# Kernel optimization log

Hardware: AMD Instinct MI355X
Metric: run time of the kernel (lower is better)

The kernel has to match this reference:

```python
import jax, jax.numpy as jnp
import numpy as np

N_NODES = 50000
N_EDGES = 800000
NF = 128   # node feature dim
EF = 64    # edge feature dim
H = 256    # hidden width (make_nn default [256, 256])
EO = 128   # edge_out_features
NO = 128   # node_out_features


def setup_inputs() -> dict:
    key = jax.random.key(0)
    ks = jax.random.split(key, 12)

    def w(k, fan_in, fan_out):
        return jax.random.normal(k, (fan_in, fan_out), jnp.float32) / np.float32(np.sqrt(fan_in))

    return {
        "node_attrs": jax.random.normal(ks[0], (N_NODES, NF), jnp.float32),
        "edge_attrs": jax.random.normal(ks[1], (N_EDGES, EF), jnp.float32),
        "senders": jax.random.randint(ks[2], (N_EDGES,), 0, N_NODES),
        "receivers": jax.random.randint(ks[3], (N_EDGES,), 0, N_NODES),
        # EdgeNet MLP: (2*NF + EF) -> 256 -> 256 -> EO
        "fe_W0": w(ks[4], 2 * NF + EF, H), "fe_b0": jnp.zeros((H,), jnp.float32),
        "fe_W1": w(ks[5], H, H),           "fe_b1": jnp.zeros((H,), jnp.float32),
        "fe_W2": w(ks[6], H, EO),          "fe_b2": jnp.zeros((EO,), jnp.float32),
        # NodeNet MLP: (NF + EO) -> 256 -> 256 -> NO
        "fn_W0": w(ks[7], NF + EO, H), "fn_b0": jnp.zeros((H,), jnp.float32),
        "fn_W1": w(ks[8], H, H),       "fn_b1": jnp.zeros((H,), jnp.float32),
        "fn_W2": w(ks[9], H, NO),      "fn_b2": jnp.zeros((NO,), jnp.float32),
    }


def _mlp(x, W0, b0, W1, b1, W2, b2):
    h = jax.nn.relu(x @ W0 + b0)
    h = jax.nn.relu(h @ W1 + b1)
    return h @ W2 + b2


def reference(node_attrs, edge_attrs, senders, receivers,
              fe_W0, fe_b0, fe_W1, fe_b1, fe_W2, fe_b2,
              fn_W0, fn_b0, fn_W1, fn_b1, fn_W2, fn_b2):
    # --- edge update: gather sender/receiver node attrs, run edge MLP ---
    ns = node_attrs[senders]     # [E, NF]
    nr = node_attrs[receivers]   # [E, NF]
    x_e = jnp.concatenate([ns, nr, edge_attrs], axis=-1)  # [E, 2*NF+EF]
    e_out = _mlp(x_e, fe_W0, fe_b0, fe_W1, fe_b1, fe_W2, fe_b2)  # [E, EO]

    # --- node update: sum incoming edge messages per receiver node ---
    in_edges = jax.ops.segment_sum(e_out, receivers, num_segments=N_NODES)  # [N, EO]
    x_n = jnp.concatenate([node_attrs, in_edges], axis=-1)  # [N, NF+EO]
    n_out = _mlp(x_n, fn_W0, fn_b0, fn_W1, fn_b1, fn_W2, fn_b2)  # [N, NO]

    # global_features == 0 -> has_global is False, g_out is empty; return node/edge outputs
    return n_out, e_out
```

## Files before the change

### kernel.cpp

```cpp
#include <hip/hip_runtime.h>

#define NNODES 50000
#define NEDGES 800000

typedef __bf16 bf16x8 __attribute__((ext_vector_type(8)));
typedef short short8 __attribute__((ext_vector_type(8)));
typedef short short4v __attribute__((ext_vector_type(4)));
typedef float f32x4 __attribute__((ext_vector_type(4)));

#define OFF_FE_W0T 0
#define OFF_FE_W1T 81920
#define OFF_FE_W2T 147456
#define OFF_FN_W0T 180224
#define OFF_FN_W1T 245760
#define OFF_FN_W2T 311296
#define OFF_CNT_B    688128
#define OFF_BASE_B   888128
#define OFF_CURSOR_B 1088384
#define OFF_EIDX_B   1288448
#define OFF_BSUM_B   4488448
#define OFF_NBF_B    4488704
#define OFF_Y_B      17288704
#define OFF_ECOPY_B  68488704
#define ECOPY_NEED   (68488704ull + 204800000ull)

__device__ __forceinline__ short f2bf(float f) {
  union { float f; unsigned u; } v; v.f = f;
  unsigned r = v.u + 0x7FFFu + ((v.u >> 16) & 1u);
  return (short)(r >> 16);
}
__device__ __forceinline__ float bf2f(short s) {
  union { unsigned u; float f; } v; v.u = ((unsigned)(unsigned short)s) << 16;
  return v.f;
}

typedef const unsigned __attribute__((address_space(1)))* gas_t;
typedef unsigned __attribute__((address_space(3)))* las_t;
__device__ __forceinline__ void gload16(const short* g, short* l) {
  __builtin_amdgcn_global_load_lds((gas_t)(const void*)g, (las_t)(void*)l, 16, 0, 0);
}

#define VMW2 asm volatile("s_waitcnt vmcnt(2)" ::: "memory")
#define VMW0 asm volatile("s_waitcnt vmcnt(0)" ::: "memory")
#define LKW0 asm volatile("s_waitcnt lgkmcnt(0)" ::: "memory")
#define BARX __builtin_amdgcn_s_barrier()
#define SBAR0 __builtin_amdgcn_sched_barrier(0)

__device__ __forceinline__ f32x4 mfma16(bf16x8 a, bf16x8 b, f32x4 c) {
  return __builtin_amdgcn_mfma_f32_16x16x32_bf16(a, b, c, 0, 0, 0);
}

template <int WTK>
__device__ __forceinline__ void stage256(const short* __restrict__ Wt, int kbase,
                                         short* slot, int wid, int lane) {
#pragma unroll
  for (int r = 0; r < 2; ++r) {
    int f = (r * 8 + wid) * 64 + lane;
    int row = f >> 2;
    int sl = f & 3;
    int sig = (row >> 1) & 3;
    const short* src = Wt + row * WTK + kbase + ((sl ^ sig) << 3);
    short* dst = slot + (r * 8 + wid) * 512;
    gload16(src, dst);
  }
}

__device__ __forceinline__ void stage128(const short* __restrict__ Wt, int kbase,
                                         short* slot, int wid, int lane) {
#pragma unroll
  for (int r = 0; r < 2; ++r) {
    int f = (r * 8 + wid) * 64 + lane;
    int row = f >> 3;
    int sl = f & 7;
    const short* src = Wt + row * 256 + kbase + ((sl ^ (row & 7)) << 3);
    short* dst = slot + (r * 8 + wid) * 512;
    gload16(src, dst);
  }
}

template <int NREP, int LDB>
__device__ __forceinline__ void comp_step(const short* xl, const short* slot, int kk,
                                          int wr, int wc, int lane, f32x4 acc[2][NREP]) {
  const int m0 = lane & 15;
  const int g = lane >> 4;
  bf16x8 a[2], b[NREP];
#pragma unroll
  for (int m = 0; m < 2; ++m) {
    int row = wr * 32 + m * 16 + m0;
    int byte = row * LDB + kk * 64 + g * 16;
    byte ^= (row & 7) << 4;
    a[m] = *(const bf16x8*)((const char*)xl + byte);
  }
#pragma unroll
  for (int n = 0; n < NREP; ++n) {
    int col = wc * (NREP * 16) + n * 16 + m0;
    int byte = col * 64 + ((g ^ ((col >> 1) & 3)) << 4);
    b[n] = *(const bf16x8*)((const char*)slot + byte);
  }
#pragma unroll
  for (int n = 0; n < NREP; ++n)
#pragma unroll
    for (int m = 0; m < 2; ++m)
      acc[m][n] = mfma16(a[m], b[n], acc[m][n]);
}

template <int LDB>
__device__ __forceinline__ void comp_pairf(const short* xl, const short* slot, int kk0,
                                           int wr, int wc, int lane, f32x4 acc[2][2]) {
  const int m0 = lane & 15;
  const int g = lane >> 4;
#pragma unroll
  for (int p = 0; p < 2; ++p) {
    const int kk = kk0 + p;
    bf16x8 a[2], b[2];
#pragma unroll
    for (int m = 0; m < 2; ++m) {
      int row = wr * 32 + m * 16 + m0;
      int byte = row * LDB + kk * 64 + g * 16;
      byte ^= (row & 7) << 4;
      a[m] = *(const bf16x8*)((const char*)xl + byte);
    }
#pragma unroll
    for (int n = 0; n < 2; ++n) {
      int col = wc * 32 + n * 16 + m0;
      int byte = col * 128 + (((p * 4 + g) ^ (col & 7)) << 4);
      b[n] = *(const bf16x8*)((const char*)slot + byte);
    }
#pragma unroll
    for (int n = 0; n < 2; ++n)
#pragma unroll
      for (int m = 0; m < 2; ++m)
        acc[m][n] = mfma16(a[m], b[n], acc[m][n]);
  }
}

template <int NREP, int LDB>
__device__ __forceinline__ void store_h2(short* xl, const float* __restrict__ bias,
                                         int wr, int wc, int lane, f32x4 acc[2][NREP]) {
  const int m0 = lane & 15;
  const int g = lane >> 4;
#pragma unroll
  for (int n = 0; n < NREP; ++n) {
    int col = wc * (NREP * 16) + n * 16 + m0;
    float bv = bias[col];
#pragma unroll
    for (int m = 0; m < 2; ++m) {
#pragma unroll
      for (int j = 0; j < 4; ++j) {
        int row = wr * 32 + m * 16 + g * 4 + j;
        float v = acc[m][n][j] + bv;
        v = fmaxf(v, 0.f);
        int byte = row * LDB + col * 2;
        byte ^= (row & 7) << 4;
        *(short*)((char*)xl + byte) = f2bf(v);
      }
    }
  }
}

__device__ __forceinline__ void store_h0_add(short* xl, const float* __restrict__ bias,
                                             int wr, int wc, int lane, f32x4 acc[2][4]) {
  const int m0 = lane & 15;
  const int g = lane >> 4;
#pragma unroll
  for (int n = 0; n < 4; ++n) {
    int col = wc * 64 + n * 16 + m0;
    float bv = bias[col];
#pragma unroll
    for (int m = 0; m < 2; ++m) {
#pragma unroll
      for (int j = 0; j < 4; ++j) {
        int row = wr * 32 + m * 16 + g * 4 + j;
        int byte = row * 512 + col * 2;
        byte ^= (row & 7) << 4;
        short* p = (short*)((char*)xl + byte);
        float v = acc[m][n][j] + bv + bf2f(*p);
        *p = f2bf(fmaxf(v, 0.f));
      }
    }
  }
}

template <typename F>
__device__ __forceinline__ void coalesced_out(float* fl, const float* __restrict__ bias,
                                              int wr, int wc, int tid, int lane,
                                              f32x4 acc[2][2], float* __restrict__ gout,
                                              short* __restrict__ ecopy, F rowmap) {
  const int m0 = lane & 15;
  const int g = lane >> 4;
#pragma unroll
  for (int n = 0; n < 2; ++n) {
    int col = wc * 32 + n * 16 + m0;
    float bv = bias[col];
#pragma unroll
    for (int m = 0; m < 2; ++m) {
#pragma unroll
      for (int j = 0; j < 4; ++j) {
        int row = wr * 32 + m * 16 + g * 4 + j;
        int byte = (row * 128 + col) * 4;
        byte ^= (row & 7) << 4;
        *(float*)((char*)fl + byte) = acc[m][n][j] + bv;
      }
    }
  }
  __syncthreads();
#pragma unroll
  for (int q = 0; q < 4; ++q) {
    int idx = q * 2048 + tid * 4;
    int row = idx >> 7;
    long grow = rowmap(row);
    if (grow < 0) continue;
    int byte = (idx * 4) ^ ((row & 7) << 4);
    float4 v = *(const float4*)((const char*)fl + byte);
    *(float4*)(gout + grow * 128 + (idx & 127)) = v;
    if (ecopy) {
      short4v pk;
      pk[0] = f2bf(v.x); pk[1] = f2bf(v.y); pk[2] = f2bf(v.z); pk[3] = f2bf(v.w);
      *(short4v*)(ecopy + grow * 128 + (idx & 127)) = pk;
    }
  }
}

__global__ __launch_bounds__(512, 4) void edge_kernel(
    const short* __restrict__ Yt, const float* __restrict__ edge_attrs,
    const int* __restrict__ senders, const int* __restrict__ receivers,
    const short* __restrict__ wsw,
    const float* __restrict__ b0, const float* __restrict__ b1,
    const float* __restrict__ b2, float* __restrict__ e_out,
    short* __restrict__ ecopy) {
  __shared__ short lds[36864];
  short* xl = lds;
  short* eal = lds + 16384;
  short* p0 = lds + 20480;
  short* p1 = lds + 28672;
  const int tid = threadIdx.x;
  const int lane = tid & 63;
  const int wid = tid >> 6;
  const int wr = wid >> 2, wc = wid & 3;
  const int e0 = blockIdx.x * 64;
  const short* w0t = wsw + OFF_FE_W0T;
  const short* w1t = wsw + OFF_FE_W1T;
  const short* w2t = wsw + OFF_FE_W2T;

  stage256<320>(w0t, 256, p0, wid, lane);

#pragma unroll
  for (int i = 0; i < 4; ++i) {
    int task = i * 512 + tid;
    int row = task >> 5;
    int c = task & 31;
    int erow = e0 + row;
    short8 vs = *(const short8*)(Yt + (size_t)senders[erow] * 512 + c * 8);
    short8 vr = *(const short8*)(Yt + (size_t)receivers[erow] * 512 + 256 + c * 8);
    short8 pk;
#pragma unroll
    for (int k = 0; k < 8; ++k) pk[k] = f2bf(bf2f(vs[k]) + bf2f(vr[k]));
    int byte = row * 512 + c * 16;
    byte ^= (row & 7) << 4;
    *(short8*)((char*)xl + byte) = pk;
  }
  {
    int row = tid >> 3;
    int c = tid & 7;
    const float* p = edge_attrs + (size_t)(e0 + row) * 64 + c * 8;
    float4 v0 = *(const float4*)p;
    float4 v1 = *(const float4*)(p + 4);
    short8 pk;
    pk[0] = f2bf(v0.x); pk[1] = f2bf(v0.y); pk[2] = f2bf(v0.z); pk[3] = f2bf(v0.w);
    pk[4] = f2bf(v1.x); pk[5] = f2bf(v1.y); pk[6] = f2bf(v1.z); pk[7] = f2bf(v1.w);
    int byte = row * 128 + c * 16;
    byte ^= (row & 7) << 4;
    *(short8*)((char*)eal + byte) = pk;
  }
  __syncthreads();

  f32x4 acc[2][4];
#pragma unroll
  for (int m = 0; m < 2; ++m)
#pragma unroll
    for (int n = 0; n < 4; ++n) acc[m][n] = (f32x4){0.f, 0.f, 0.f, 0.f};
  f32x4 acc2[2][2];
#pragma unroll
  for (int m = 0; m < 2; ++m)
#pragma unroll
    for (int n = 0; n < 2; ++n) acc2[m][n] = (f32x4){0.f, 0.f, 0.f, 0.f};

#pragma unroll
  for (int t = 0; t < 14; ++t) {
    if (t == 2) {
      store_h0_add(xl, b0, wr, wc, lane, acc);
      SBAR0; LKW0; SBAR0; BARX; SBAR0;
#pragma unroll
      for (int m = 0; m < 2; ++m)
#pragma unroll
        for (int n = 0; n < 4; ++n) acc[m][n] = (f32x4){0.f, 0.f, 0.f, 0.f};
    }
    if (t == 10) {
      store_h2<4, 512>(xl, b1, wr, wc, lane, acc);
      SBAR0; LKW0; SBAR0; BARX; SBAR0;
    }
    if (t < 13) {
      const int u = t + 1;
      short* nxt = (u & 1) ? p1 : p0;
      if (u <= 1)      stage256<320>(w0t, 256 + u * 32, nxt, wid, lane);
      else if (u <= 9) stage256<256>(w1t, (u - 2) * 32, nxt, wid, lane);
      else             stage128(w2t, (u - 10) * 64, nxt, wid, lane);
    }
    SBAR0;
    if (t < 13) { VMW2; } else { VMW0; }
    SBAR0; BARX; SBAR0;
    const short* cur = (t & 1) ? p1 : p0;
    if (t < 2)       comp_step<4, 128>(eal, cur, t, wr, wc, lane, acc);
    else if (t < 10) comp_step<4, 512>(xl, cur, t - 2, wr, wc, lane, acc);
    else             comp_pairf<512>(xl, cur, (t - 10) * 2, wr, wc, lane, acc2);
    SBAR0; BARX; SBAR0;
  }

  coalesced_out((float*)lds, b2, wr, wc, tid, lane, acc2, e_out, ecopy,
                [&](int row) -> long { return (long)(e0 + row); });
}

template <int KSTEPS, int MF, int NREP, int LDB, int WTK>
__device__ __forceinline__ void gemm_layer(const short* lds, const short* Wt,
                                           int wn, int lane, f32x4 acc[MF][NREP]) {
  const int m0 = lane & 15;
  const int g = lane >> 4;
  const short* wp = Wt + (wn * (NREP * 16) + m0) * WTK + g * 8;
  bf16x8 bcur[NREP], bnxt[NREP], a[MF];
#pragma unroll
  for (int n = 0; n < NREP; ++n) bcur[n] = *(const bf16x8*)(wp + n * 16 * WTK);
#pragma unroll
  for (int ks = 0; ks < KSTEPS; ++ks) {
    if (ks + 1 < KSTEPS) {
#pragma unroll
      for (int n = 0; n < NREP; ++n)
        bnxt[n] = *(const bf16x8*)(wp + (ks + 1) * 32 + n * 16 * WTK);
    }
    const int kb = ks * 32 + g * 8;
#pragma unroll
    for (int m = 0; m < MF; ++m) {
      int row = m * 16 + m0;
      int byte = row * LDB + kb * 2;
      byte ^= (row & 7) << 4;
      a[m] = *(const bf16x8*)((const char*)lds + byte);
    }
#pragma unroll
    for (int n = 0; n < NREP; ++n)
#pragma unroll
      for (int m = 0; m < MF; ++m)
        acc[m][n] = __builtin_amdgcn_mfma_f32_16x16x32_bf16(a[m], bcur[n], acc[m][n], 0, 0, 0);
#pragma unroll
    for (int n = 0; n < NREP; ++n) bcur[n] = bnxt[n];
  }
}

template <int MF, int NREP, int LDB>
__device__ __forceinline__ void store_h(short* lds, const float* __restrict__ bias,
                                        int wn, int lane, f32x4 acc[MF][NREP]) {
  const int m0 = lane & 15;
  const int g = lane >> 4;
#pragma unroll
  for (int n = 0; n < NREP; ++n) {
    int col = wn * (NREP * 16) + n * 16 + m0;
    float bv = bias[col];
#pragma unroll
    for (int m = 0; m < MF; ++m) {
#pragma unroll
      for (int j = 0; j < 4; ++j) {
        int row = m * 16 + g * 4 + j;
        float v = acc[m][n][j] + bv;
        v = fmaxf(v, 0.f);
        int byte = row * LDB + col * 2;
        byte ^= (row & 7) << 4;
        *(short*)((char*)lds + byte) = f2bf(v);
      }
    }
  }
}

__global__ __launch_bounds__(512, 2) void yprep_kernel(
    const short* __restrict__ nbf, const short* __restrict__ w0t,
    short* __restrict__ Y) {
  __shared__ short lds[40960];
  short* xs = lds;
  short* yl = lds + 8192;
  const int tid = threadIdx.x;
  const int lane = tid & 63;
  const int wn = tid >> 6;
  const int n0 = blockIdx.x * 64;

#pragma unroll
  for (int i = 0; i < 2; ++i) {
    int task = i * 512 + tid;
    int row = task >> 4;
    int c = task & 15;
    int nrow = n0 + row;
    if (nrow >= NNODES) nrow = NNODES - 1;
    short8 pk = *(const short8*)(nbf + (size_t)nrow * 128 + c * 8);
    int byte = row * 256 + c * 16;
    byte ^= (row & 7) << 4;
    *(short8*)((char*)xs + byte) = pk;
  }
  __syncthreads();

  f32x4 acc[4][4];
#pragma unroll
  for (int m = 0; m < 4; ++m)
#pragma unroll
    for (int n = 0; n < 4; ++n) acc[m][n] = (f32x4){0.f, 0.f, 0.f, 0.f};
  gemm_layer<4, 4, 4, 256, 320>(xs, w0t + (wn >> 2) * 128, wn & 3, lane, acc);

  const int m0 = lane & 15;
  const int g = lane >> 4;
  const int colbase = (wn & 3) * 64 + (wn >> 2) * 256;
#pragma unroll
  for (int n = 0; n < 4; ++n) {
    int col = colbase + n * 16 + m0;
#pragma unroll
    for (int m = 0; m < 4; ++m)
#pragma unroll
      for (int j = 0; j < 4; ++j) {
        int row = m * 16 + g * 4 + j;
        yl[row * 512 + col] = f2bf(acc[m][n][j]);
      }
  }
  __syncthreads();

#pragma unroll
  for (int i = 0; i < 8; ++i) {
    int idx = i * 512 + tid;
    int row = idx >> 6;
    int c = idx & 63;
    int nrow = n0 + row;
    if (nrow >= NNODES) continue;
    *(short8*)(Y + (size_t)nrow * 512 + c * 8) = *(const short8*)(yl + row * 512 + c * 8);
  }
}

__global__ __launch_bounds__(512, 4) void node_kernel(
    const short* __restrict__ nbf, const float* __restrict__ e_out,
    const short* __restrict__ ecopy,
    const int* __restrict__ basep, const int* __restrict__ eidx,
    const short* __restrict__ wsw,
    const float* __restrict__ b0, const float* __restrict__ b1,
    const float* __restrict__ b2, float* __restrict__ n_out) {
  __shared__ short lds[16384];
  const int tid = threadIdx.x;
  const int lane = tid & 63;
  const int wn = tid >> 6;
  const int r0 = blockIdx.x * 64;

#pragma unroll
  for (int i = 0; i < 2; ++i) {
    int task = i * 512 + tid;
    int row = task >> 4;
    int c = task & 15;
    int nrow = r0 + row;
    if (nrow >= NNODES) nrow = NNODES - 1;
    short8 pk = *(const short8*)(nbf + (size_t)nrow * 128 + c * 8);
    int byte = row * 512 + c * 16;
    byte ^= (row & 7) << 4;
    *(short8*)((char*)lds + byte) = pk;
  }

  {
    const int n_local = tid >> 3;
    const int cg = tid & 7;
    const int node = r0 + n_local;
    float sum[16];
#pragma unroll
    for (int q = 0; q < 16; ++q) sum[q] = 0.f;
    if (node < NNODES) {
      int beg = basep[node], end = basep[node + 1];
      if (ecopy) {
        for (int j = beg; j < end; ++j) {
          int e = eidx[j];
          const short8* er = (const short8*)(ecopy + (size_t)e * 128 + cg * 16);
          short8 v0 = er[0], v1 = er[1];
#pragma unroll
          for (int k = 0; k < 8; ++k) {
            sum[k] += bf2f(v0[k]);
            sum[8 + k] += bf2f(v1[k]);
          }
        }
      } else {
        for (int j = beg; j < end; ++j) {
          int e = eidx[j];
          const float* er = e_out + (size_t)e * 128 + cg * 16;
#pragma unroll
          for (int q = 0; q < 4; ++q) {
            float4 v = *(const float4*)(er + q * 4);
            sum[q * 4 + 0] += v.x; sum[q * 4 + 1] += v.y;
            sum[q * 4 + 2] += v.z; sum[q * 4 + 3] += v.w;
          }
        }
      }
    }
#pragma unroll
    for (int q = 0; q < 2; ++q) {
      short8 pk;
#pragma unroll
      for (int k = 0; k < 8; ++k) pk[k] = f2bf(sum[q * 8 + k]);
      int col = 128 + cg * 16 + q * 8;
      int byte = n_local * 512 + col * 2;
      byte ^= (n_local & 7) << 4;
      *(short8*)((char*)lds + byte) = pk;
    }
  }
  __syncthreads();

  f32x4 acc[4][2];
#pragma unroll
  for (int m = 0; m < 4; ++m)
#pragma unroll
    for (int n = 0; n < 2; ++n) acc[m][n] = (f32x4){0.f, 0.f, 0.f, 0.f};
  gemm_layer<8, 4, 2, 512, 256>(lds, wsw + OFF_FN_W0T, wn, lane, acc);
  __syncthreads();
  store_h<4, 2, 512>(lds, b0, wn, lane, acc);
  __syncthreads();

#pragma unroll
  for (int m = 0; m < 4; ++m)
#pragma unroll
    for (int n = 0; n < 2; ++n) acc[m][n] = (f32x4){0.f, 0.f, 0.f, 0.f};
  gemm_layer<8, 4, 2, 512, 256>(lds, wsw + OFF_FN_W1T, wn, lane, acc);
  __syncthreads();
  store_h<4, 2, 512>(lds, b1, wn, lane, acc);
  __syncthreads();

  f32x4 acc2[4][1];
#pragma unroll
  for (int m = 0; m < 4; ++m) acc2[m][0] = (f32x4){0.f, 0.f, 0.f, 0.f};
  gemm_layer<8, 4, 1, 512, 256>(lds, wsw + OFF_FN_W2T, wn, lane, acc2);
  __syncthreads();

  {
    float* fl = (float*)lds;
    const int m0 = lane & 15;
    const int g = lane >> 4;
    int col = wn * 16 + m0;
    float bv = b2[col];
#pragma unroll
    for (int m = 0; m < 4; ++m) {
#pragma unroll
      for (int j = 0; j < 4; ++j) {
        int row = m * 16 + g * 4 + j;
        int byte = (row * 128 + col) * 4;
        byte ^= (row & 7) << 4;
        *(float*)((char*)fl + byte) = acc2[m][0][j] + bv;
      }
    }
    __syncthreads();
#pragma unroll
    for (int q = 0; q < 4; ++q) {
      int idx = q * 2048 + tid * 4;
      int row = idx >> 7;
      long grow = r0 + row;
      if (grow >= NNODES) continue;
      int byte = (idx * 4) ^ ((row & 7) << 4);
      float4 v = *(const float4*)((const char*)fl + byte);
      *(float4*)(n_out + grow * 128 + (idx & 127)) = v;
    }
  }
}

__global__ void prep_weights_all(const float* __restrict__ w0, const float* __restrict__ w1,
                                 const float* __restrict__ w2, const float* __restrict__ w3,
                                 const float* __restrict__ w4, const float* __restrict__ w5,
                                 short* __restrict__ wsw) {
  const float* src; short* dst; int K, N;
  switch (blockIdx.y) {
    case 0: src = w0; dst = wsw + OFF_FE_W0T; K = 320; N = 256; break;
    case 1: src = w1; dst = wsw + OFF_FE_W1T; K = 256; N = 256; break;
    case 2: src = w2; dst = wsw + OFF_FE_W2T; K = 256; N = 128; break;
    case 3: src = w3; dst = wsw + OFF_FN_W0T; K = 256; N = 256; break;
    case 4: src = w4; dst = wsw + OFF_FN_W1T; K = 256; N = 256; break;
    default: src = w5; dst = wsw + OFF_FN_W2T; K = 256; N = 128; break;
  }
  int idx = blockIdx.x * 256 + threadIdx.x;
  if (idx < K * N) {
    int k = idx / N;
    int n = idx - k * N;
    dst[n * K + k] = f2bf(src[idx]);
  }
}

__global__ void cvt_bf16(const float* __restrict__ src, short* __restrict__ dst, int n8) {
  int i = blockIdx.x * 256 + threadIdx.x;
  if (i < n8) {
    float4 v0 = ((const float4*)src)[i * 2];
    float4 v1 = ((const float4*)src)[i * 2 + 1];
    short8 pk;
    pk[0] = f2bf(v0.x); pk[1] = f2bf(v0.y); pk[2] = f2bf(v0.z); pk[3] = f2bf(v0.w);
    pk[4] = f2bf(v1.x); pk[5] = f2bf(v1.y); pk[6] = f2bf(v1.z); pk[7] = f2bf(v1.w);
    ((short8*)dst)[i] = pk;
  }
}

__global__ void hist_kernel(const int* __restrict__ receivers, int* __restrict__ cnt) {
  int e = blockIdx.x * 512 + threadIdx.x;
  if (e < NEDGES) atomicAdd(&cnt[receivers[e]], 1);
}

__global__ __launch_bounds__(1024) void scan1_kernel(const int* __restrict__ cnt,
                                                     int* __restrict__ base,
                                                     int* __restrict__ bsum) {
  __shared__ int s[1024];
  const int tid = threadIdx.x;
  int i = blockIdx.x * 1024 + tid;
  int v = (i < NNODES) ? cnt[i] : 0;
  s[tid] = v;
  __syncthreads();
  for (int off = 1; off < 1024; off <<= 1) {
    int t = (tid >= off) ? s[tid - off] : 0;
    __syncthreads();
    s[tid] += t;
    __syncthreads();
  }
  if (i < NNODES) base[i] = s[tid] - v;
  if (tid == 1023) bsum[blockIdx.x] = s[1023];
}

__global__ void scan2_kernel(int* __restrict__ bsum, int nblk) {
  if (threadIdx.x == 0) {
    int run = 0;
    for (int b = 0; b < nblk; ++b) { int t = bsum[b]; bsum[b] = run; run += t; }
  }
}

__global__ __launch_bounds__(1024) void scan3_kernel(const int* __restrict__ bsum,
                                                     int* __restrict__ base,
                                                     int* __restrict__ cursor) {
  int i = blockIdx.x * 1024 + threadIdx.x;
  if (i < NNODES) {
    int b = base[i] + bsum[blockIdx.x];
    base[i] = b;
    cursor[i] = b;
  }
  if (i == 0) base[NNODES] = NEDGES;
}

__global__ void scatter_kernel(const int* __restrict__ receivers, int* __restrict__ cursor,
                               int* __restrict__ eidx) {
  int e = blockIdx.x * 512 + threadIdx.x;
  if (e < NEDGES) {
    int pos = atomicAdd(&cursor[receivers[e]], 1);
    eidx[pos] = e;
  }
}

extern "C" void kernel_launch(void* const* d_in, const int* in_sizes, int n_in,
                              void* d_out, int out_size, void* d_ws, size_t ws_size,
                              hipStream_t stream) {
  const float* node_attrs = (const float*)d_in[0];
  const float* edge_attrs = (const float*)d_in[1];
  const int* senders = (const int*)d_in[2];
  const int* receivers = (const int*)d_in[3];
  const float* fe_W0 = (const float*)d_in[4];
  const float* fe_b0 = (const float*)d_in[5];
  const float* fe_W1 = (const float*)d_in[6];
  const float* fe_b1 = (const float*)d_in[7];
  const float* fe_W2 = (const float*)d_in[8];
  const float* fe_b2 = (const float*)d_in[9];
  const float* fn_W0 = (const float*)d_in[10];
  const float* fn_b0 = (const float*)d_in[11];
  const float* fn_W1 = (const float*)d_in[12];
  const float* fn_b1 = (const float*)d_in[13];
  const float* fn_W2 = (const float*)d_in[14];
  const float* fn_b2 = (const float*)d_in[15];

  short* wsw  = (short*)d_ws;
  int* cnt    = (int*)((char*)d_ws + OFF_CNT_B);
  int* basep  = (int*)((char*)d_ws + OFF_BASE_B);
  int* cursor = (int*)((char*)d_ws + OFF_CURSOR_B);
  int* eidx   = (int*)((char*)d_ws + OFF_EIDX_B);
  int* bsum   = (int*)((char*)d_ws + OFF_BSUM_B);
  short* nbf  = (short*)((char*)d_ws + OFF_NBF_B);
  short* Yt   = (short*)((char*)d_ws + OFF_Y_B);
  short* ecopy = (ws_size >= ECOPY_NEED) ? (short*)((char*)d_ws + OFF_ECOPY_B) : nullptr;
  float* out = (float*)d_out;
  float* n_out = out;
  float* e_out = out + (size_t)NNODES * 128;

  dim3 gprep(320, 6);
  prep_weights_all<<<gprep, 256, 0, stream>>>(fe_W0, fe_W1, fe_W2, fn_W0, fn_W1, fn_W2, wsw);
  cvt_bf16<<<(NNODES * 128 / 8 + 255) / 256, 256, 0, stream>>>(node_attrs, nbf, NNODES * 128 / 8);
  hipMemsetAsync(cnt, 0, NNODES * sizeof(int), stream);

  yprep_kernel<<<(NNODES + 63) / 64, 512, 0, stream>>>(nbf, wsw + OFF_FE_W0T, Yt);

  const int nscan = (NNODES + 1023) / 1024;
  hist_kernel<<<(NEDGES + 511) / 512, 512, 0, stream>>>(receivers, cnt);
  scan1_kernel<<<nscan, 1024, 0, stream>>>(cnt, basep, bsum);
  scan2_kernel<<<1, 64, 0, stream>>>(bsum, nscan);
  scan3_kernel<<<nscan, 1024, 0, stream>>>(bsum, basep, cursor);
  scatter_kernel<<<(NEDGES + 511) / 512, 512, 0, stream>>>(receivers, cursor, eidx);

  edge_kernel<<<NEDGES / 64, 512, 0, stream>>>(Yt, edge_attrs, senders, receivers,
                                               wsw, fe_b0, fe_b1, fe_b2, e_out, ecopy);
  node_kernel<<<(NNODES + 63) / 64, 512, 0, stream>>>(nbf, e_out, ecopy, basep, eidx, wsw,
                                                      fn_b0, fn_b1, fn_b2, n_out);
}
```

Baseline: 728.2 us.

## Triple-buffer edge weight staging and keep edge attributes in registers

The edge kernel's weight-slab pipeline moves from double to triple buffering. Staging now runs two steps ahead, which removes one of the two block barriers per step; the remaining barriers move around the hidden-layer stores. Edge attributes are loaded straight into MFMA A-operand registers in bf16 instead of going through a shared-memory tile. This cuts barrier and LDS traffic, but LDS use grows to 80KB per block and register pressure rises, which may lower occupancy under the 4-blocks launch bound.

```diff
diff --git a/kernel.cpp b/kernel.cpp
--- a/kernel.cpp
+++ b/kernel.cpp
@@ -34,6 +34,13 @@
   return v.f;
 }
 
+__device__ __forceinline__ bf16x8 pack8(float4 a, float4 b) {
+  union { short8 s; bf16x8 h; } u;
+  u.s[0] = f2bf(a.x); u.s[1] = f2bf(a.y); u.s[2] = f2bf(a.z); u.s[3] = f2bf(a.w);
+  u.s[4] = f2bf(b.x); u.s[5] = f2bf(b.y); u.s[6] = f2bf(b.z); u.s[7] = f2bf(b.w);
+  return u.h;
+}
+
 typedef const unsigned __attribute__((address_space(1)))* gas_t;
 typedef unsigned __attribute__((address_space(3)))* las_t;
 __device__ __forceinline__ void gload16(const short* g, short* l) {
@@ -102,6 +109,25 @@
 #pragma unroll
     for (int m = 0; m < 2; ++m)
       acc[m][n] = mfma16(a[m], b[n], acc[m][n]);
+}
+
+template <int NREP>
+__device__ __forceinline__ void comp_rega(bf16x8 a0, bf16x8 a1, const short* slot,
+                                          int wc, int lane, f32x4 acc[2][NREP]) {
+  const int m0 = lane & 15;
+  const int g = lane >> 4;
+  bf16x8 b[NREP];
+#pragma unroll
+  for (int n = 0; n < NREP; ++n) {
+    int col = wc * (NREP * 16) + n * 16 + m0;
+    int byte = col * 64 + ((g ^ ((col >> 1) & 3)) << 4);
+    b[n] = *(const bf16x8*)((const char*)slot + byte);
+  }
+#pragma unroll
+  for (int n = 0; n < NREP; ++n) {
+    acc[0][n] = mfma16(a0, b[n], acc[0][n]);
+    acc[1][n] = mfma16(a1, b[n], acc[1][n]);
+  }
 }
 
 template <int LDB>
@@ -228,11 +254,9 @@
     const float* __restrict__ b0, const float* __restrict__ b1,
     const float* __restrict__ b2, float* __restrict__ e_out,
     short* __restrict__ ecopy) {
-  __shared__ short lds[36864];
+  __shared__ short lds[40960];
   short* xl = lds;
-  short* eal = lds + 16384;
-  short* p0 = lds + 20480;
-  short* p1 = lds + 28672;
+  short* q[3] = {lds + 16384, lds + 24576, lds + 32768};
   const int tid = threadIdx.x;
   const int lane = tid & 63;
   const int wid = tid >> 6;
@@ -242,7 +266,8 @@
   const short* w1t = wsw + OFF_FE_W1T;
   const short* w2t = wsw + OFF_FE_W2T;
 
-  stage256<320>(w0t, 256, p0, wid, lane);
+  stage256<320>(w0t, 256, q[0], wid, lane);
+  stage256<320>(w0t, 288, q[1], wid, lane);
 
 #pragma unroll
   for (int i = 0; i < 4; ++i) {
@@ -259,18 +284,19 @@
     byte ^= (row & 7) << 4;
     *(short8*)((char*)xl + byte) = pk;
   }
+
+  bf16x8 ea0[2], ea1[2];
   {
-    int row = tid >> 3;
-    int c = tid & 7;
-    const float* p = edge_attrs + (size_t)(e0 + row) * 64 + c * 8;
-    float4 v0 = *(const float4*)p;
-    float4 v1 = *(const float4*)(p + 4);
-    short8 pk;
-    pk[0] = f2bf(v0.x); pk[1] = f2bf(v0.y); pk[2] = f2bf(v0.z); pk[3] = f2bf(v0.w);
-    pk[4] = f2bf(v1.x); pk[5] = f2bf(v1.y); pk[6] = f2bf(v1.z); pk[7] = f2bf(v1.w);
-    int byte = row * 128 + c * 16;
-    byte ^= (row & 7) << 4;
-    *(short8*)((char*)eal + byte) = pk;
+    const int m0 = lane & 15;
+    const int g = lane >> 4;
+#pragma unroll
+    for (int m = 0; m < 2; ++m) {
+      size_t row = (size_t)(e0 + wr * 32 + m * 16 + m0);
+      const float* pa = edge_attrs + row * 64 + g * 8;
+      ea0[m] = pack8(*(const float4*)pa, *(const float4*)(pa + 4));
+      const float* pb = edge_attrs + row * 64 + 32 + g * 8;
+      ea1[m] = pack8(*(const float4*)pb, *(const float4*)(pb + 4));
+    }
   }
   __syncthreads();
 
@@ -289,32 +315,35 @@
   for (int t = 0; t < 14; ++t) {
     if (t == 2) {
       store_h0_add(xl, b0, wr, wc, lane, acc);
-      SBAR0; LKW0; SBAR0; BARX; SBAR0;
+      SBAR0; LKW0; SBAR0;
 #pragma unroll
       for (int m = 0; m < 2; ++m)
 #pragma unroll
         for (int n = 0; n < 4; ++n) acc[m][n] = (f32x4){0.f, 0.f, 0.f, 0.f};
     }
     if (t == 10) {
+      SBAR0; BARX; SBAR0;
       store_h2<4, 512>(xl, b1, wr, wc, lane, acc);
-      SBAR0; LKW0; SBAR0; BARX; SBAR0;
-    }
-    if (t < 13) {
-      const int u = t + 1;
-      short* nxt = (u & 1) ? p1 : p0;
-      if (u <= 1)      stage256<320>(w0t, 256 + u * 32, nxt, wid, lane);
-      else if (u <= 9) stage256<256>(w1t, (u - 2) * 32, nxt, wid, lane);
-      else             stage128(w2t, (u - 10) * 64, nxt, wid, lane);
+      SBAR0; LKW0; SBAR0;
     }
     SBAR0;
-    if (t < 13) { VMW2; } else { VMW0; }
+    if (t <= 12) { VMW2; } else { VMW0; }
     SBAR0; BARX; SBAR0;
-    const short* cur = (t & 1) ? p1 : p0;
-    if (t < 2)       comp_step<4, 128>(eal, cur, t, wr, wc, lane, acc);
+    if (t + 2 <= 13) {
+      const int u = t + 2;
+      short* nxt = q[u % 3];
+      if (u <= 9) stage256<256>(w1t, (u - 2) * 32, nxt, wid, lane);
+      else        stage128(w2t, (u - 10) * 64, nxt, wid, lane);
+    }
+    SBAR0;
+    const short* cur = q[t % 3];
+    if (t == 0)      comp_rega<4>(ea0[0], ea0[1], cur, wc, lane, acc);
+    else if (t == 1) comp_rega<4>(ea1[0], ea1[1], cur, wc, lane, acc);
     else if (t < 10) comp_step<4, 512>(xl, cur, t - 2, wr, wc, lane, acc);
     else             comp_pairf<512>(xl, cur, (t - 10) * 2, wr, wc, lane, acc2);
-    SBAR0; BARX; SBAR0;
-  }
+    SBAR0;
+  }
+  SBAR0; BARX; SBAR0;
 
   coalesced_out((float*)lds, b2, wr, wc, tid, lane, acc2, e_out, ecopy,
                 [&](int row) -> long { return (long)(e0 + row); });
```

New measurement: 796.3 us. 9.4% more time.
